# Optimization experiments

Hardware: AMD Instinct MI355X
Metric: run time of the kernel (lower is better)

The kernel has to match this reference:

```python
import jax, jax.numpy as jnp
import numpy as np

N = 50000          # nodes
E = 800000         # edges
IN = 32            # in_channels (train_tensor.shape[1])
OUT = 256          # out_channels
K = 4              # Chebyshev order
LAMBDA_MAX = 2.0   # canonical lambda_max for sym-normalized Laplacian


def setup_inputs() -> dict:
    key = jax.random.key(0)
    ks = jax.random.split(key, 32)
    inp = {}
    inp["X"] = jax.random.normal(ks[0], (N, IN), jnp.float32)
    inp["edge_index"] = jax.random.randint(ks[1], (2, E), 0, N)
    inp["edge_weight"] = jax.random.uniform(ks[2], (E,), jnp.float32)
    inp["H"] = jax.random.normal(ks[3], (N, OUT), jnp.float32)
    inp["C"] = jax.random.normal(ks[4], (N, OUT), jnp.float32)
    i = 5
    s_in = float(np.sqrt(6.0 / (IN + OUT)))   # glorot for W_g
    s_ch = float(np.sqrt(1.0 / OUT))          # ChebConv linear init scale
    for g in ["i", "f", "c", "o"]:
        inp[f"W_{g}"] = jax.random.uniform(ks[i], (IN, OUT), jnp.float32, -s_in, s_in); i += 1
        inp[f"b_{g}"] = jnp.zeros((1, OUT), jnp.float32)
        inp[f"conv_{g}_w"] = jax.random.uniform(ks[i], (K, OUT, OUT), jnp.float32, -s_ch, s_ch); i += 1
        inp[f"conv_{g}_b"] = jnp.zeros((OUT,), jnp.float32)
    return inp


def _cheb_basis(H, edge_index, edge_weight, lam):
    """Chebyshev basis T_0(L~)H .. T_{K-1}(L~)H for the scaled sym Laplacian.
    L~ = (2/lam) * (I - D^{-1/2} A D^{-1/2}) - I  (PyG ChebConv.__norm__)."""
    n = H.shape[0]
    src, dst = edge_index[0], edge_index[1]
    deg = jax.ops.segment_sum(edge_weight, src, num_segments=n)
    dis = jnp.where(deg > 0, jax.lax.rsqrt(deg), 0.0)
    w = -(2.0 / lam) * dis[src] * edge_weight * dis[dst]   # scaled off-diagonal
    d = 2.0 / lam - 1.0                                     # scaled diagonal

    def prop(x):  # L~ @ x via edge scatter + diagonal
        return jax.ops.segment_sum(w[:, None] * x[src], dst, num_segments=n) + d * x

    Tx0 = H
    Tx1 = prop(Tx0)
    Tx2 = 2.0 * prop(Tx1) - Tx0
    Tx3 = 2.0 * prop(Tx2) - Tx1
    return jnp.stack([Tx0, Tx1, Tx2, Tx3])  # [K, N, OUT]


def reference(X, edge_index, edge_weight, H, C,
              W_i, b_i, conv_i_w, conv_i_b,
              W_f, b_f, conv_f_w, conv_f_b,
              W_c, b_c, conv_c_w, conv_c_b,
              W_o, b_o, conv_o_w, conv_o_b):
    # Shared Chebyshev basis of H (identical across the 4 gates)
    Tx = _cheb_basis(H, edge_index, edge_weight, LAMBDA_MAX)  # [K, N, OUT]

    def gate(Wg, bg, cw, cb):
        conv = jnp.einsum('knf,kfo->no', Tx, cw) + cb
        return X @ Wg + conv + bg

    I = jax.nn.sigmoid(gate(W_i, b_i, conv_i_w, conv_i_b))
    F = jax.nn.sigmoid(gate(W_f, b_f, conv_f_w, conv_f_b))
    T = jnp.tanh(gate(W_c, b_c, conv_c_w, conv_c_b))
    C_new = F * C + I * T
    O = jax.nn.sigmoid(gate(W_o, b_o, conv_o_w, conv_o_b))
    H_new = O * jnp.tanh(C_new)
    return (H_new, C_new)
```

## Files before the change

### kernel.cpp

```cpp
#include <hip/hip_runtime.h>
#include <math.h>

#define NN   50000
#define EE   800000
#define INC  32
#define OUTC 256
#define NKB  132

using bf16x8 = __attribute__((ext_vector_type(8))) short;
using u16x8  = __attribute__((ext_vector_type(8))) unsigned short;
using f32x4  = __attribute__((ext_vector_type(4))) float;

struct __align__(8) Edge { int s; float w; };

__device__ __forceinline__ unsigned short f2b(float f) {
  union { float f; unsigned u; } v; v.f = f;
  return (unsigned short)((v.u + 0x7FFFu + ((v.u >> 16) & 1u)) >> 16);
}
__device__ __forceinline__ float b2f(unsigned short u) {
  union { unsigned u; float f; } v; v.u = ((unsigned)u) << 16; return v.f;
}


__global__ void k_edge1(const int* __restrict__ ei, const float* __restrict__ ew,
                        float* __restrict__ deg, int* __restrict__ cnt) {
  for (int e = blockIdx.x * blockDim.x + threadIdx.x; e < EE;
       e += gridDim.x * blockDim.x) {
    atomicAdd(&deg[ei[e]], ew[e]);
    atomicAdd(&cnt[ei[EE + e]], 1);
  }
}

__global__ __launch_bounds__(512) void k_scan1(const int* __restrict__ cnt,
                                               int* __restrict__ row_ptr,
                                               int* __restrict__ bsum) {
  __shared__ int sd[512];
  int t = threadIdx.x;
  int i = blockIdx.x * 512 + t;
  int x = (i < NN) ? cnt[i] : 0;
  sd[t] = x;
  __syncthreads();
  for (int off = 1; off < 512; off <<= 1) {
    int v = (t >= off) ? sd[t - off] : 0;
    __syncthreads();
    sd[t] += v;
    __syncthreads();
  }
  if (i < NN) row_ptr[i] = sd[t] - x;
  if (t == 511) bsum[blockIdx.x] = sd[511];
}

__global__ __launch_bounds__(128) void k_scan2(int* __restrict__ bsum,
                                               int* __restrict__ row_ptr,
                                               int nblk) {
  __shared__ int sd[128];
  int t = threadIdx.x;
  int x = (t < nblk) ? bsum[t] : 0;
  sd[t] = x;
  __syncthreads();
  for (int off = 1; off < 128; off <<= 1) {
    int v = (t >= off) ? sd[t - off] : 0;
    __syncthreads();
    sd[t] += v;
    __syncthreads();
  }
  if (t < nblk) bsum[t] = sd[t] - x;
  if (t == 127) row_ptr[NN] = sd[127];
}

__global__ void k_scan3(int* __restrict__ row_ptr, const int* __restrict__ bsum,
                        int* __restrict__ nxt, float* __restrict__ deg) {
  int i = blockIdx.x * blockDim.x + threadIdx.x;
  if (i < NN) {
    int v = row_ptr[i] + bsum[i >> 9];
    row_ptr[i] = v;
    nxt[i] = v;
    float d = deg[i];
    deg[i] = d > 0.f ? rsqrtf(d) : 0.f;
  }
}

__global__ void k_fill(const int* __restrict__ ei, const float* __restrict__ ew,
                       const float* __restrict__ dis, int* __restrict__ nxt,
                       Edge* __restrict__ ev) {
  for (int e = blockIdx.x * blockDim.x + threadIdx.x; e < EE;
       e += gridDim.x * blockDim.x) {
    int s = ei[e], d = ei[EE + e];
    int pos = atomicAdd(&nxt[d], 1);
    Edge eg; eg.s = s; eg.w = -dis[s] * ew[e] * dis[d];
    ev[pos] = eg;
  }
}


__global__ __launch_bounds__(256) void k_prop_bf(
    const int* __restrict__ row_ptr, const Edge* __restrict__ ev,
    const unsigned short* __restrict__ xb,
    const unsigned short* __restrict__ initb, float scale,
    unsigned short* __restrict__ outb, unsigned short* __restrict__ apk) {
  int wid = blockIdx.x * 4 + (threadIdx.x >> 6);
  if (wid >= NN) return;
  int lane = threadIdx.x & 63;
  int half = lane >> 5;
  int cl = lane & 31;
  int start = __builtin_amdgcn_readfirstlane(row_ptr[wid]);
  int end = __builtin_amdgcn_readfirstlane(row_ptr[wid + 1]);
  const size_t cofs = (size_t)(cl << 3);

  float a0[8], a1[8], a2[8], a3[8];
#pragma unroll
  for (int i = 0; i < 8; ++i) { a0[i] = 0.f; a1[i] = 0.f; a2[i] = 0.f; a3[i] = 0.f; }

  int j = start;
  for (; j + 7 < end; j += 8) {
    Edge e0 = ev[j + half];
    Edge e1 = ev[j + 2 + half];
    Edge e2 = ev[j + 4 + half];
    Edge e3 = ev[j + 6 + half];
    u16x8 u0 = *(const u16x8*)(xb + (size_t)e0.s * OUTC + cofs);
    u16x8 u1 = *(const u16x8*)(xb + (size_t)e1.s * OUTC + cofs);
    u16x8 u2 = *(const u16x8*)(xb + (size_t)e2.s * OUTC + cofs);
    u16x8 u3 = *(const u16x8*)(xb + (size_t)e3.s * OUTC + cofs);
#pragma unroll
    for (int i = 0; i < 8; ++i) {
      a0[i] = fmaf(e0.w, b2f(u0[i]), a0[i]);
      a1[i] = fmaf(e1.w, b2f(u1[i]), a1[i]);
      a2[i] = fmaf(e2.w, b2f(u2[i]), a2[i]);
      a3[i] = fmaf(e3.w, b2f(u3[i]), a3[i]);
    }
  }
  for (; j + 1 < end; j += 2) {
    Edge e0 = ev[j + half];
    u16x8 u0 = *(const u16x8*)(xb + (size_t)e0.s * OUTC + cofs);
#pragma unroll
    for (int i = 0; i < 8; ++i) a0[i] = fmaf(e0.w, b2f(u0[i]), a0[i]);
  }
  if (j < end) {
    Edge e0 = ev[j];
    float wv = half ? 0.f : e0.w;
    u16x8 u0 = *(const u16x8*)(xb + (size_t)e0.s * OUTC + cofs);
#pragma unroll
    for (int i = 0; i < 8; ++i) a0[i] = fmaf(wv, b2f(u0[i]), a0[i]);
  }

  float o[8];
#pragma unroll
  for (int i = 0; i < 8; ++i) {
    float s = (a0[i] + a1[i]) + (a2[i] + a3[i]);
    s += __shfl_xor(s, 32);
    o[i] = s;
  }
  if (initb) {
    u16x8 iv = *(const u16x8*)(initb + (size_t)wid * OUTC + cofs);
#pragma unroll
    for (int i = 0; i < 8; ++i) o[i] = scale * o[i] - b2f(iv[i]);
  }
  u16x8 h;
#pragma unroll
  for (int i = 0; i < 8; ++i) h[i] = f2b(o[i]);
  if (half == 0) {
    *(u16x8*)(apk + ((size_t)cl * NN + wid) * 8) = h;
  } else if (outb) {
    *(u16x8*)(outb + (size_t)wid * OUTC + cofs) = h;
  }
}


__global__ void k_packXH(const float* __restrict__ X, const float* __restrict__ H,
                         unsigned short* __restrict__ apk,
                         unsigned short* __restrict__ hrm) {
  int t = blockIdx.x * blockDim.x + threadIdx.x;
  if (t < NN * 4) {
    int row = t >> 2, kb = t & 3;
    float4 a = *(const float4*)(X + (size_t)row * INC + kb * 8);
    float4 b = *(const float4*)(X + (size_t)row * INC + kb * 8 + 4);
    u16x8 h;
    h[0] = f2b(a.x); h[1] = f2b(a.y); h[2] = f2b(a.z); h[3] = f2b(a.w);
    h[4] = f2b(b.x); h[5] = f2b(b.y); h[6] = f2b(b.z); h[7] = f2b(b.w);
    *(u16x8*)(apk + ((size_t)kb * NN + row) * 8) = h;
  } else if (t < NN * 36) {
    int u = t - NN * 4;
    int row = u >> 5, kb = u & 31;
    float4 a = *(const float4*)(H + (size_t)row * OUTC + kb * 8);
    float4 b = *(const float4*)(H + (size_t)row * OUTC + kb * 8 + 4);
    u16x8 h;
    h[0] = f2b(a.x); h[1] = f2b(a.y); h[2] = f2b(a.z); h[3] = f2b(a.w);
    h[4] = f2b(b.x); h[5] = f2b(b.y); h[6] = f2b(b.z); h[7] = f2b(b.w);
    *(u16x8*)(apk + ((size_t)(kb + 4) * NN + row) * 8) = h;
    *(u16x8*)(hrm + (size_t)row * OUTC + kb * 8) = h;
  }
}

struct BPtrs {
  const float* W[4];
  const float* cw[4];
  const float* b[4];
  const float* cb[4];
};

__global__ void k_packB(BPtrs bp, unsigned short* __restrict__ bpk,
                        float* __restrict__ bias_pk) {
  int t = blockIdx.x * blockDim.x + threadIdx.x;
  if (t >= NKB * 1024) return;
  int kb = t >> 10, p = t & 1023;
  int j = p >> 8, c = (p >> 6) & 3, g = (p >> 4) & 3, s = p & 15;
  int o = j * 64 + c * 16 + s;
  u16x8 h;
#pragma unroll
  for (int j8 = 0; j8 < 8; ++j8) {
    int k = kb * 8 + j8;
    float v = (k < 32) ? bp.W[g][k * OUTC + o]
                       : bp.cw[g][(size_t)(k - 32) * OUTC + o];
    h[j8] = f2b(v);
  }
  *(u16x8*)(bpk + (size_t)t * 8) = h;
  if (kb == 0) bias_pk[p] = bp.b[g][o] + bp.cb[g][o];
}


__device__ __forceinline__ float sigf(float x) {
  return __builtin_amdgcn_rcpf(1.0f + __expf(-x));
}
__device__ __forceinline__ float tanhfast(float x) {
  float e = __expf(2.0f * x);
  return 1.0f - 2.0f * __builtin_amdgcn_rcpf(e + 1.0f);
}

#define AS1(p) ((__attribute__((address_space(1))) void*)(p))
#define AS3(p) ((__attribute__((address_space(3))) void*)(p))

__global__ __launch_bounds__(512, 4) void k_gemm_mfma(
    const unsigned short* __restrict__ Apk,
    const unsigned short* __restrict__ Bpk,
    const float* __restrict__ bias_pk,
    const float* __restrict__ C,
    float* __restrict__ Hn, float* __restrict__ Cn) {
  __shared__ unsigned short Als[3][4 * 128 * 8];
  __shared__ unsigned short Bls[3][4 * 256 * 8];

  const int b = blockIdx.x;
  const int xcd = b & 7;
  const int slot = b >> 3;
  const int cgrp = slot & 3;
  const int rblk = xcd + ((slot >> 2) << 3);
  const int bm0 = rblk * 128;
  if (bm0 >= NN) return;
  const int cb0 = cgrp * 256;

  const int tid = threadIdx.x;
  const int lane = tid & 63;
  const int wid = tid >> 6;
  const int wr = wid >> 2;
  const int wc = wid & 3;

  f32x4 acc[4][4];
#pragma unroll
  for (int i = 0; i < 4; ++i)
#pragma unroll
    for (int j = 0; j < 4; ++j) acc[i][j] = (f32x4){0.f, 0.f, 0.f, 0.f};

  int a_row = bm0 + ((wid & 1) << 6) + lane;
  if (a_row > NN - 1) a_row = NN - 1;
  const unsigned short* aG = Apk + ((size_t)(wid >> 1) * NN + a_row) * 8;
  const int idx0 = wid << 6;
  const int idx1 = 512 + (wid << 6);
  const unsigned short* bG0 =
      Bpk + (((size_t)(idx0 >> 8)) * 1024 + cb0 + (idx0 & 255) + lane) * 8;
  const unsigned short* bG1 =
      Bpk + (((size_t)(idx1 >> 8)) * 1024 + cb0 + (idx1 & 255) + lane) * 8;

  auto STAGE_A = [&](int buf, int tile) {
    __builtin_amdgcn_global_load_lds(AS1(aG + ((size_t)(tile << 2)) * NN * 8),
                                     AS3(&Als[buf][(wid << 6) * 8]), 16, 0, 0);
  };
  auto STAGE_B = [&](int buf, int tile) {
    const size_t kofs = (size_t)(tile << 2);
    __builtin_amdgcn_global_load_lds(AS1(bG0 + kofs * 1024 * 8),
                                     AS3(&Bls[buf][idx0 * 8]), 16, 0, 0);
    __builtin_amdgcn_global_load_lds(AS1(bG1 + kofs * 1024 * 8),
                                     AS3(&Bls[buf][idx1 * 8]), 16, 0, 0);
  };

  const int koff = lane >> 4;
  const int r15 = lane & 15;
  const int NT = NKB / 4;

  STAGE_A(0, 0); STAGE_B(0, 0);
  STAGE_A(1, 1); STAGE_B(1, 1);
  int cur = 0;
  for (int t = 0; t < NT; ++t) {
    if (t < NT - 1)
      asm volatile("s_waitcnt vmcnt(3)\n\ts_barrier" ::: "memory");
    else
      asm volatile("s_waitcnt vmcnt(0)\n\ts_barrier" ::: "memory");

    const unsigned short* Ab = &Als[cur][((koff << 7) + (wr << 6) + r15) * 8];
    const unsigned short* Bb = &Bls[cur][((koff << 8) + (wc << 6) + r15) * 8];

    bf16x8 af0 = *(const bf16x8*)(Ab + 0 * 128);
    bf16x8 af1 = *(const bf16x8*)(Ab + 16 * 8);
    bf16x8 af2 = *(const bf16x8*)(Ab + 32 * 8);
    bf16x8 af3 = *(const bf16x8*)(Ab + 48 * 8);
    bf16x8 bf0 = *(const bf16x8*)(Bb + 0 * 8);
    bf16x8 bf1 = *(const bf16x8*)(Bb + 16 * 8);
    if (t + 2 < NT) STAGE_A((t + 2) % 3, t + 2);
    __builtin_amdgcn_s_barrier();
    asm volatile("s_waitcnt lgkmcnt(0)" ::: "memory");
    __builtin_amdgcn_sched_barrier(0);
    __builtin_amdgcn_s_setprio(1);
    acc[0][0] = __builtin_amdgcn_mfma_f32_16x16x32_bf16(af0, bf0, acc[0][0], 0, 0, 0);
    acc[1][0] = __builtin_amdgcn_mfma_f32_16x16x32_bf16(af1, bf0, acc[1][0], 0, 0, 0);
    acc[2][0] = __builtin_amdgcn_mfma_f32_16x16x32_bf16(af2, bf0, acc[2][0], 0, 0, 0);
    acc[3][0] = __builtin_amdgcn_mfma_f32_16x16x32_bf16(af3, bf0, acc[3][0], 0, 0, 0);
    acc[0][1] = __builtin_amdgcn_mfma_f32_16x16x32_bf16(af0, bf1, acc[0][1], 0, 0, 0);
    acc[1][1] = __builtin_amdgcn_mfma_f32_16x16x32_bf16(af1, bf1, acc[1][1], 0, 0, 0);
    acc[2][1] = __builtin_amdgcn_mfma_f32_16x16x32_bf16(af2, bf1, acc[2][1], 0, 0, 0);
    acc[3][1] = __builtin_amdgcn_mfma_f32_16x16x32_bf16(af3, bf1, acc[3][1], 0, 0, 0);
    __builtin_amdgcn_s_setprio(0);

    bf16x8 bf2 = *(const bf16x8*)(Bb + 32 * 8);
    bf16x8 bf3 = *(const bf16x8*)(Bb + 48 * 8);
    if (t + 2 < NT) STAGE_B((t + 2) % 3, t + 2);
    __builtin_amdgcn_s_barrier();
    asm volatile("s_waitcnt lgkmcnt(0)" ::: "memory");
    __builtin_amdgcn_sched_barrier(0);
    __builtin_amdgcn_s_setprio(1);
    acc[0][2] = __builtin_amdgcn_mfma_f32_16x16x32_bf16(af0, bf2, acc[0][2], 0, 0, 0);
    acc[1][2] = __builtin_amdgcn_mfma_f32_16x16x32_bf16(af1, bf2, acc[1][2], 0, 0, 0);
    acc[2][2] = __builtin_amdgcn_mfma_f32_16x16x32_bf16(af2, bf2, acc[2][2], 0, 0, 0);
    acc[3][2] = __builtin_amdgcn_mfma_f32_16x16x32_bf16(af3, bf2, acc[3][2], 0, 0, 0);
    acc[0][3] = __builtin_amdgcn_mfma_f32_16x16x32_bf16(af0, bf3, acc[0][3], 0, 0, 0);
    acc[1][3] = __builtin_amdgcn_mfma_f32_16x16x32_bf16(af1, bf3, acc[1][3], 0, 0, 0);
    acc[2][3] = __builtin_amdgcn_mfma_f32_16x16x32_bf16(af2, bf3, acc[2][3], 0, 0, 0);
    acc[3][3] = __builtin_amdgcn_mfma_f32_16x16x32_bf16(af3, bf3, acc[3][3], 0, 0, 0);
    __builtin_amdgcn_s_setprio(0);

    cur = (cur + 1 == 3) ? 0 : cur + 1;
  }

  const int ocol = cgrp * 64 + (wc << 4) + r15;
  float bz[4];
#pragma unroll
  for (int g = 0; g < 4; ++g) bz[g] = bias_pk[cb0 + (wc << 6) + (g << 4) + r15];

#pragma unroll
  for (int mi = 0; mi < 4; ++mi) {
    int rowb = bm0 + (wr << 6) + (mi << 4) + ((lane >> 4) << 2);
#pragma unroll
    for (int q = 0; q < 4; ++q) {
      int r = rowb + q;
      if (r >= NN) continue;
      float zi = acc[mi][0][q] + bz[0];
      float zf = acc[mi][1][q] + bz[1];
      float zc = acc[mi][2][q] + bz[2];
      float zo = acc[mi][3][q] + bz[3];
      float cold = C[(size_t)r * OUTC + ocol];
      float I = sigf(zi), F = sigf(zf), T = tanhfast(zc), O = sigf(zo);
      float cn = fmaf(F, cold, I * T);
      Cn[(size_t)r * OUTC + ocol] = cn;
      Hn[(size_t)r * OUTC + ocol] = O * tanhfast(cn);
    }
  }
}


extern "C" void kernel_launch(void* const* d_in, const int* in_sizes, int n_in,
                              void* d_out, int out_size, void* d_ws, size_t ws_size,
                              hipStream_t stream) {
  const float* X = (const float*)d_in[0];
  const int* EI = (const int*)d_in[1];
  const float* EW = (const float*)d_in[2];
  const float* H = (const float*)d_in[3];
  const float* C = (const float*)d_in[4];

  char* ws = (char*)d_ws;
  size_t off = 0;
  auto alloc = [&](size_t bytes) -> void* {
    void* p = ws + off;
    off += (bytes + 255) & ~(size_t)255;
    return p;
  };
  int* row_ptr = (int*)alloc((NN + 1) * sizeof(int));
  int* cnt = (int*)alloc(NN * sizeof(int));
  int* nextp = (int*)alloc(NN * sizeof(int));
  int* bsum = (int*)alloc(128 * sizeof(int));
  Edge* ev = (Edge*)alloc(EE * sizeof(Edge));
  float* dis = (float*)alloc(NN * sizeof(float));
  unsigned short* Hrm = (unsigned short*)alloc((size_t)NN * OUTC * sizeof(unsigned short));
  unsigned short* T1rm = (unsigned short*)alloc((size_t)NN * OUTC * sizeof(unsigned short));
  unsigned short* T2rm = (unsigned short*)alloc((size_t)NN * OUTC * sizeof(unsigned short));
  unsigned short* Apk = (unsigned short*)alloc((size_t)NKB * NN * 8 * sizeof(unsigned short));
  unsigned short* Bpk = (unsigned short*)alloc((size_t)NKB * 1024 * 8 * sizeof(unsigned short));
  float* bias_pk = (float*)alloc(1024 * sizeof(float));
  (void)ws_size; (void)in_sizes; (void)n_in; (void)out_size;

  hipMemsetAsync(dis, 0, NN * sizeof(float), stream);
  hipMemsetAsync(cnt, 0, NN * sizeof(int), stream);

  const int ge = 1024;
  k_edge1<<<ge, 256, 0, stream>>>(EI, EW, dis, cnt);
  const int nscb = (NN + 511) / 512;
  k_scan1<<<nscb, 512, 0, stream>>>(cnt, row_ptr, bsum);
  k_scan2<<<1, 128, 0, stream>>>(bsum, row_ptr, nscb);
  k_scan3<<<(NN + 255) / 256, 256, 0, stream>>>(row_ptr, bsum, nextp, dis);
  k_fill<<<ge, 256, 0, stream>>>(EI, EW, dis, nextp, ev);

  k_packXH<<<(NN * 36 + 255) / 256, 256, 0, stream>>>(X, H, Apk, Hrm);
  BPtrs bp;
  for (int g = 0; g < 4; ++g) {
    bp.W[g] = (const float*)d_in[5 + 4 * g];
    bp.b[g] = (const float*)d_in[6 + 4 * g];
    bp.cw[g] = (const float*)d_in[7 + 4 * g];
    bp.cb[g] = (const float*)d_in[8 + 4 * g];
  }
  k_packB<<<(NKB * 1024 + 255) / 256, 256, 0, stream>>>(bp, Bpk, bias_pk);

  const int pgrid = (NN + 3) / 4;
  k_prop_bf<<<pgrid, 256, 0, stream>>>(row_ptr, ev, Hrm, nullptr, 1.f,
                                       T1rm, Apk + (size_t)36 * NN * 8);
  k_prop_bf<<<pgrid, 256, 0, stream>>>(row_ptr, ev, T1rm, Hrm, 2.f,
                                       T2rm, Apk + (size_t)68 * NN * 8);
  k_prop_bf<<<pgrid, 256, 0, stream>>>(row_ptr, ev, T2rm, T1rm, 2.f,
                                       nullptr, Apk + (size_t)100 * NN * 8);

  float* Hn = (float*)d_out;
  float* Cn = (float*)d_out + (size_t)NN * OUTC;
  k_gemm_mfma<<<8 * 49 * 4, 512, 0, stream>>>(Apk, Bpk, bias_pk, C, Hn, Cn);
}
```

Measured before the change: 501.5 us.

## Halve GEMM column tile to 128 and merge per-iteration barrier phases

Shrinks the fused gate GEMM's B tile from 256 to 128 packed columns (32 output channels × 4 gates) per block, doubling the grid and halving per-wave accumulators and LDS. B packing is re-laid out to match, and the two half-iteration load/barrier phases are merged into one phase per K-tile. The aim is higher occupancy (launch bound raised to 6 blocks) and fewer barriers, at the cost of re-reading each A tile twice as often and having less MFMA work per LDS load.

```diff
diff --git a/kernel.cpp b/kernel.cpp
--- a/kernel.cpp
+++ b/kernel.cpp
@@ -203,8 +203,8 @@
   int t = blockIdx.x * blockDim.x + threadIdx.x;
   if (t >= NKB * 1024) return;
   int kb = t >> 10, p = t & 1023;
-  int j = p >> 8, c = (p >> 6) & 3, g = (p >> 4) & 3, s = p & 15;
-  int o = j * 64 + c * 16 + s;
+  int j = p >> 7, c = (p >> 6) & 1, g = (p >> 4) & 3, s = p & 15;
+  int o = j * 32 + c * 16 + s;
   u16x8 h;
 #pragma unroll
   for (int j8 = 0; j8 < 8; ++j8) {
@@ -229,56 +229,50 @@
 #define AS1(p) ((__attribute__((address_space(1))) void*)(p))
 #define AS3(p) ((__attribute__((address_space(3))) void*)(p))
 
-__global__ __launch_bounds__(512, 4) void k_gemm_mfma(
+__global__ __launch_bounds__(512, 6) void k_gemm_mfma(
     const unsigned short* __restrict__ Apk,
     const unsigned short* __restrict__ Bpk,
     const float* __restrict__ bias_pk,
     const float* __restrict__ C,
     float* __restrict__ Hn, float* __restrict__ Cn) {
   __shared__ unsigned short Als[3][4 * 128 * 8];
-  __shared__ unsigned short Bls[3][4 * 256 * 8];
+  __shared__ unsigned short Bls[3][4 * 128 * 8];
 
   const int b = blockIdx.x;
   const int xcd = b & 7;
   const int slot = b >> 3;
-  const int cgrp = slot & 3;
-  const int rblk = xcd + ((slot >> 2) << 3);
+  const int cgrp = slot & 7;
+  const int rblk = xcd + ((slot >> 3) << 3);
   const int bm0 = rblk * 128;
   if (bm0 >= NN) return;
-  const int cb0 = cgrp * 256;
+  const int cb0 = cgrp * 128;
 
   const int tid = threadIdx.x;
   const int lane = tid & 63;
   const int wid = tid >> 6;
-  const int wr = wid >> 2;
-  const int wc = wid & 3;
-
-  f32x4 acc[4][4];
-#pragma unroll
-  for (int i = 0; i < 4; ++i)
+  const int wr = wid >> 1;
+  const int wc = wid & 1;
+
+  f32x4 acc[2][4];
+#pragma unroll
+  for (int i = 0; i < 2; ++i)
 #pragma unroll
     for (int j = 0; j < 4; ++j) acc[i][j] = (f32x4){0.f, 0.f, 0.f, 0.f};
 
   int a_row = bm0 + ((wid & 1) << 6) + lane;
   if (a_row > NN - 1) a_row = NN - 1;
   const unsigned short* aG = Apk + ((size_t)(wid >> 1) * NN + a_row) * 8;
-  const int idx0 = wid << 6;
-  const int idx1 = 512 + (wid << 6);
-  const unsigned short* bG0 =
-      Bpk + (((size_t)(idx0 >> 8)) * 1024 + cb0 + (idx0 & 255) + lane) * 8;
-  const unsigned short* bG1 =
-      Bpk + (((size_t)(idx1 >> 8)) * 1024 + cb0 + (idx1 & 255) + lane) * 8;
+  const int idxw = wid << 6;
+  const unsigned short* bG =
+      Bpk + (((size_t)(idxw >> 7)) * 1024 + cb0 + (idxw & 127) + lane) * 8;
 
   auto STAGE_A = [&](int buf, int tile) {
     __builtin_amdgcn_global_load_lds(AS1(aG + ((size_t)(tile << 2)) * NN * 8),
                                      AS3(&Als[buf][(wid << 6) * 8]), 16, 0, 0);
   };
   auto STAGE_B = [&](int buf, int tile) {
-    const size_t kofs = (size_t)(tile << 2);
-    __builtin_amdgcn_global_load_lds(AS1(bG0 + kofs * 1024 * 8),
-                                     AS3(&Bls[buf][idx0 * 8]), 16, 0, 0);
-    __builtin_amdgcn_global_load_lds(AS1(bG1 + kofs * 1024 * 8),
-                                     AS3(&Bls[buf][idx1 * 8]), 16, 0, 0);
+    __builtin_amdgcn_global_load_lds(AS1(bG + ((size_t)(tile << 2)) * 1024 * 8),
+                                     AS3(&Bls[buf][(wid << 6) * 8]), 16, 0, 0);
   };
 
   const int koff = lane >> 4;
@@ -290,62 +284,45 @@
   int cur = 0;
   for (int t = 0; t < NT; ++t) {
     if (t < NT - 1)
-      asm volatile("s_waitcnt vmcnt(3)\n\ts_barrier" ::: "memory");
+      asm volatile("s_waitcnt vmcnt(2)\n\ts_barrier" ::: "memory");
     else
       asm volatile("s_waitcnt vmcnt(0)\n\ts_barrier" ::: "memory");
 
-    const unsigned short* Ab = &Als[cur][((koff << 7) + (wr << 6) + r15) * 8];
-    const unsigned short* Bb = &Bls[cur][((koff << 8) + (wc << 6) + r15) * 8];
-
-    bf16x8 af0 = *(const bf16x8*)(Ab + 0 * 128);
+    const unsigned short* Ab = &Als[cur][((koff << 7) + (wr << 5) + r15) * 8];
+    const unsigned short* Bb = &Bls[cur][((koff << 7) + (wc << 6) + r15) * 8];
+
+    bf16x8 af0 = *(const bf16x8*)(Ab + 0 * 8);
     bf16x8 af1 = *(const bf16x8*)(Ab + 16 * 8);
-    bf16x8 af2 = *(const bf16x8*)(Ab + 32 * 8);
-    bf16x8 af3 = *(const bf16x8*)(Ab + 48 * 8);
     bf16x8 bf0 = *(const bf16x8*)(Bb + 0 * 8);
     bf16x8 bf1 = *(const bf16x8*)(Bb + 16 * 8);
-    if (t + 2 < NT) STAGE_A((t + 2) % 3, t + 2);
+    bf16x8 bf2 = *(const bf16x8*)(Bb + 32 * 8);
+    bf16x8 bf3 = *(const bf16x8*)(Bb + 48 * 8);
+    if (t + 2 < NT) { STAGE_A((t + 2) % 3, t + 2); STAGE_B((t + 2) % 3, t + 2); }
     __builtin_amdgcn_s_barrier();
     asm volatile("s_waitcnt lgkmcnt(0)" ::: "memory");
     __builtin_amdgcn_sched_barrier(0);
     __builtin_amdgcn_s_setprio(1);
     acc[0][0] = __builtin_amdgcn_mfma_f32_16x16x32_bf16(af0, bf0, acc[0][0], 0, 0, 0);
     acc[1][0] = __builtin_amdgcn_mfma_f32_16x16x32_bf16(af1, bf0, acc[1][0], 0, 0, 0);
-    acc[2][0] = __builtin_amdgcn_mfma_f32_16x16x32_bf16(af2, bf0, acc[2][0], 0, 0, 0);
-    acc[3][0] = __builtin_amdgcn_mfma_f32_16x16x32_bf16(af3, bf0, acc[3][0], 0, 0, 0);
     acc[0][1] = __builtin_amdgcn_mfma_f32_16x16x32_bf16(af0, bf1, acc[0][1], 0, 0, 0);
     acc[1][1] = __builtin_amdgcn_mfma_f32_16x16x32_bf16(af1, bf1, acc[1][1], 0, 0, 0);
-    acc[2][1] = __builtin_amdgcn_mfma_f32_16x16x32_bf16(af2, bf1, acc[2][1], 0, 0, 0);
-    acc[3][1] = __builtin_amdgcn_mfma_f32_16x16x32_bf16(af3, bf1, acc[3][1], 0, 0, 0);
-    __builtin_amdgcn_s_setprio(0);
-
-    bf16x8 bf2 = *(const bf16x8*)(Bb + 32 * 8);
-    bf16x8 bf3 = *(const bf16x8*)(Bb + 48 * 8);
-    if (t + 2 < NT) STAGE_B((t + 2) % 3, t + 2);
-    __builtin_amdgcn_s_barrier();
-    asm volatile("s_waitcnt lgkmcnt(0)" ::: "memory");
-    __builtin_amdgcn_sched_barrier(0);
-    __builtin_amdgcn_s_setprio(1);
     acc[0][2] = __builtin_amdgcn_mfma_f32_16x16x32_bf16(af0, bf2, acc[0][2], 0, 0, 0);
     acc[1][2] = __builtin_amdgcn_mfma_f32_16x16x32_bf16(af1, bf2, acc[1][2], 0, 0, 0);
-    acc[2][2] = __builtin_amdgcn_mfma_f32_16x16x32_bf16(af2, bf2, acc[2][2], 0, 0, 0);
-    acc[3][2] = __builtin_amdgcn_mfma_f32_16x16x32_bf16(af3, bf2, acc[3][2], 0, 0, 0);
     acc[0][3] = __builtin_amdgcn_mfma_f32_16x16x32_bf16(af0, bf3, acc[0][3], 0, 0, 0);
     acc[1][3] = __builtin_amdgcn_mfma_f32_16x16x32_bf16(af1, bf3, acc[1][3], 0, 0, 0);
-    acc[2][3] = __builtin_amdgcn_mfma_f32_16x16x32_bf16(af2, bf3, acc[2][3], 0, 0, 0);
-    acc[3][3] = __builtin_amdgcn_mfma_f32_16x16x32_bf16(af3, bf3, acc[3][3], 0, 0, 0);
     __builtin_amdgcn_s_setprio(0);
 
     cur = (cur + 1 == 3) ? 0 : cur + 1;
   }
 
-  const int ocol = cgrp * 64 + (wc << 4) + r15;
+  const int ocol = cgrp * 32 + (wc << 4) + r15;
   float bz[4];
 #pragma unroll
   for (int g = 0; g < 4; ++g) bz[g] = bias_pk[cb0 + (wc << 6) + (g << 4) + r15];
 
 #pragma unroll
-  for (int mi = 0; mi < 4; ++mi) {
-    int rowb = bm0 + (wr << 6) + (mi << 4) + ((lane >> 4) << 2);
+  for (int mi = 0; mi < 2; ++mi) {
+    int rowb = bm0 + (wr << 5) + (mi << 4) + ((lane >> 4) << 2);
 #pragma unroll
     for (int q = 0; q < 4; ++q) {
       int r = rowb + q;
@@ -425,5 +402,5 @@
 
   float* Hn = (float*)d_out;
   float* Cn = (float*)d_out + (size_t)NN * OUTC;
-  k_gemm_mfma<<<8 * 49 * 4, 512, 0, stream>>>(Apk, Bpk, bias_pk, C, Hn, Cn);
-}
+  k_gemm_mfma<<<8 * 49 * 8, 512, 0, stream>>>(Apk, Bpk, bias_pk, C, Hn, Cn);
+}
```

New measurement: 495.4 us. Within noise of the previous version (-1.2%).
